# Kernel optimization log

Hardware: AMD Instinct MI355X
Metric: run time of the kernel (lower is better)

Reference implementation:

```python
import jax, jax.numpy as jnp
import numpy as np

B, S, D, H, C, E, V = 8, 2048, 1024, 512, 256, 64, 64


def setup_inputs() -> dict:
    key = jax.random.key(0)
    ks = jax.random.split(key, 40)
    ri = lambda i, hi: jax.random.randint(ks[i], (B, S), 0, hi).astype(jnp.int32)
    p = lambda i, shape: (jax.random.normal(ks[i], shape, jnp.float32) * 0.02)
    inp = {
        'h_x': jax.random.normal(ks[0], (B, S, D), jnp.float32),
        'h_y': jax.random.normal(ks[1], (B, S, D), jnp.float32),
        'x_mask': jnp.ones((B, S), jnp.int32),
        'y_mask': jnp.ones((B, S), jnp.int32),
        'src_token_dense_mask': ri(2, 2), 'src_token_sparse_mask': ri(3, 2),
        'src_token_inarc_type': ri(4, V), 'src_token_arc_head': ri(5, S),
        'src_token_depth': ri(6, 16), 'src_word_inarc_type': ri(7, V),
        'src_word_inarc_type_mask': ri(8, 2),
        'tgt_token_dense_mask': ri(9, 2), 'tgt_token_sparse_mask': ri(10, 2),
        'tgt_token_inarc_type': ri(11, V), 'tgt_token_arc_head': ri(12, S),
        'tgt_token_depth': ri(13, 16), 'tgt_word_inarc_type': ri(14, V),
        'tgt_word_inarc_type_mask': ri(15, 2),
        # src MLP [D->H->C], tgt MLP [D->H->C]
        'W1s': p(16, (D, H)), 'b1s': jnp.zeros((H,), jnp.float32),
        'W2s': p(17, (H, C)), 'b2s': jnp.zeros((C,), jnp.float32),
        'W1t': p(18, (D, H)), 'b1t': jnp.zeros((H,), jnp.float32),
        'W2t': p(19, (H, C)), 'b2t': jnp.zeros((C,), jnp.float32),
        # inarc edge embedding + GeneralConv params
        'emb': p(20, (V, E)),
        'W_msg': p(21, (C, C)), 'b_msg': jnp.zeros((C,), jnp.float32),
        'W_edge': p(22, (E, C)),
        'att': p(23, (C,)),
        'W_self': p(24, (C, C)), 'b_self': jnp.zeros((C,), jnp.float32),
        # axis_feature MLP [C->C]
        'Wf': p(25, (C, C)), 'bf': jnp.zeros((C,), jnp.float32),
    }
    return inp


def _mlp(h, W1, b1, W2, b2):
    return jax.nn.leaky_relu(h @ W1 + b1) @ W2 + b2


def _graph_side(h, dense_m, sparse_m, arc_head, word_type, word_mask,
                W1, b1, W2, b2, emb, W_msg, b_msg, W_edge, att, W_self, b_self, Wf, bf):
    Bn, Sn, _ = h.shape
    x = _mlp(h, W1, b1, W2, b2)                      # [B,S,C]
    N = Bn * Sn
    Cn = x.shape[-1]
    xg = x.reshape(N, Cn)                            # debatch -> nodes
    off = (jnp.arange(Bn, dtype=jnp.int32) * Sn)[:, None]
    src = (arc_head + off).reshape(N)                # global head index per token
    dst = jnp.arange(N, dtype=jnp.int32)             # one in-edge per token
    valid = (sparse_m * dense_m).reshape(N).astype(x.dtype)
    ef = emb[(word_type * word_mask).reshape(N)]     # [N,E] edge embeddings
    # GeneralConv: directed message with edge features + additive attention
    m = xg[src] @ W_msg + b_msg + ef @ W_edge        # [N,C] messages
    hd = xg @ W_msg + b_msg                          # dst-side term for attention
    logit = jax.nn.leaky_relu(((m + hd) * att).sum(-1))
    logit = jnp.where(valid > 0, logit, -1e9)
    emax = jax.ops.segment_max(logit, dst, num_segments=N)
    ex = jnp.exp(logit - emax[dst]) * valid
    den = jax.ops.segment_sum(ex, dst, num_segments=N)
    alpha = ex / (den[dst] + 1e-16)                  # softmax per destination node
    agg = jax.ops.segment_sum(m * alpha[:, None], dst, num_segments=N)
    out = xg @ W_self + b_self + agg                 # skip_linear
    out = out / jnp.maximum(jnp.linalg.norm(out, axis=-1, keepdims=True), 1e-12)
    r = out.reshape(Bn, Sn, Cn).mean(axis=1, keepdims=True)  # FeatureRepr mean
    return r @ Wf + bf                               # [B,1,C]


def reference(h_x, x_mask, src_token_dense_mask, src_token_sparse_mask,
              src_token_inarc_type, src_token_arc_head, src_token_depth,
              src_word_inarc_type, src_word_inarc_type_mask,
              h_y, y_mask, tgt_token_dense_mask, tgt_token_sparse_mask,
              tgt_token_inarc_type, tgt_token_arc_head, tgt_token_depth,
              tgt_word_inarc_type, tgt_word_inarc_type_mask,
              W1s, b1s, W2s, b2s, W1t, b1t, W2t, b2t,
              emb, W_msg, b_msg, W_edge, att, W_self, b_self, Wf, bf):
    src_repr = _graph_side(h_x, src_token_dense_mask, src_token_sparse_mask,
                           src_token_arc_head, src_word_inarc_type, src_word_inarc_type_mask,
                           W1s, b1s, W2s, b2s, emb, W_msg, b_msg, W_edge, att,
                           W_self, b_self, Wf, bf)
    tgt_repr = _graph_side(h_y, tgt_token_dense_mask, tgt_token_sparse_mask,
                           tgt_token_arc_head, tgt_word_inarc_type, tgt_word_inarc_type_mask,
                           W1t, b1t, W2t, b2t, emb, W_msg, b_msg, W_edge, att,
                           W_self, b_self, Wf, bf)
    return (src_repr, tgt_repr)
```

## Files before the change

kernel.cpp:

```cpp
#include <hip/hip_runtime.h>
#include <stdint.h>

#define SEQ   2048
#define NNODE 16384

typedef short  short8  __attribute__((ext_vector_type(8)));
typedef float  float4v __attribute__((ext_vector_type(4)));
typedef unsigned short u16;
typedef unsigned short u16x8 __attribute__((ext_vector_type(8)));
typedef short  short4v __attribute__((ext_vector_type(4)));

__device__ __forceinline__ float b2f(u16 u) {
    union { unsigned int i; float f; } x; x.i = ((unsigned int)u) << 16; return x.f;
}
__device__ __forceinline__ u16 f2b(float f) {
    union { float f; unsigned int i; } x; x.f = f;
    unsigned int u = x.i;
    unsigned int r = (u + 0x7fffu + ((u >> 16) & 1u)) >> 16;
    return (u16)r;
}

__device__ __forceinline__ void gld16(const void* g, void* l) {
    __builtin_amdgcn_global_load_lds(
        (const __attribute__((address_space(1))) void*)g,
        (__attribute__((address_space(3))) void*)l, 16, 0, 0);
}

struct GemmP {
    const void*  A[2];
    const u16*   B[2];
    const float* bias[2];
    u16*         out[2];
};

#define LDW 136

template <int ACT, int AF32>
__global__ __launch_bounds__(256, 2) void gemm_k(GemmP p, int M, int N, int K) {
    __shared__ __align__(16) u16 smem[32768];

    const int z = blockIdx.z;
    const u16*   __restrict__ B    = p.B[z];
    const float* __restrict__ bias = p.bias[z];
    const u16*   __restrict__ A16  = (const u16*)p.A[z];
    const float* __restrict__ A32  = (const float*)p.A[z];

    const int mt  = blockIdx.x * 128;
    const int nt  = blockIdx.y * 128;
    const int tid = threadIdx.x;
    const int l   = tid & 63;
    const int w   = tid >> 6;
    const int wm  = (w >> 1) * 64;
    const int wn  = (w & 1) * 64;
    const int lr  = l & 15;
    const int lk  = l >> 4;

    float4v acc[4][4] = {};
    float4v pa[8];

    auto stageB = [&](int k0, u16* Bs) {
#pragma unroll
        for (int it = 0; it < 4; ++it) {
            int f = it * 256 + tid, rm = f >> 3, cc = f & 7, gc = cc ^ (rm & 7);
            gld16(B + (size_t)(nt + rm) * K + (k0 + gc * 8), Bs + (size_t)f * 8);
        }
    };
    auto stageA16 = [&](int k0, u16* As) {
#pragma unroll
        for (int it = 0; it < 4; ++it) {
            int f = it * 256 + tid, rm = f >> 3, cc = f & 7, gc = cc ^ (rm & 7);
            gld16(A16 + (size_t)(mt + rm) * K + (k0 + gc * 8), As + (size_t)f * 8);
        }
    };
    auto prefA32 = [&](int k0) {
#pragma unroll
        for (int it = 0; it < 4; ++it) {
            int f = it * 256 + tid, rm = f >> 3, cc = f & 7;
            const float* s = A32 + (size_t)(mt + rm) * K + k0 + cc * 8;
            pa[2 * it]     = *(const float4v*)s;
            pa[2 * it + 1] = *(const float4v*)(s + 4);
        }
    };
    auto cvtWrite = [&](u16* As) {
#pragma unroll
        for (int it = 0; it < 4; ++it) {
            int f = it * 256 + tid, rm = f >> 3, cc = f & 7;
            float4v a = pa[2 * it], b = pa[2 * it + 1];
            u16x8 r;
            r[0] = f2b(a[0]); r[1] = f2b(a[1]); r[2] = f2b(a[2]); r[3] = f2b(a[3]);
            r[4] = f2b(b[0]); r[5] = f2b(b[1]); r[6] = f2b(b[2]); r[7] = f2b(b[3]);
            *(u16x8*)(As + ((size_t)rm * 8 + (cc ^ (rm & 7))) * 8) = r;
        }
    };

    const int niter = K >> 6;

    if (AF32) { prefA32(0); cvtWrite(smem); }
    else      { stageA16(0, smem); }
    stageB(0, smem + 8192);
    __syncthreads();

    for (int ki = 0; ki < niter; ++ki) {
        u16* curb = smem + (ki & 1) * 16384;
        u16* nxtb = smem + ((ki & 1) ^ 1) * 16384;
        const bool more = (ki + 1) < niter;
        if (more) {
            if (AF32) prefA32((ki + 1) * 64);
            else      stageA16((ki + 1) * 64, nxtb);
            stageB((ki + 1) * 64, nxtb + 8192);
        }
        const u16* As = curb;
        const u16* Bs = curb + 8192;
#pragma unroll
        for (int ks = 0; ks < 2; ++ks) {
            short8 af[4], bfr[4];
            const int kc = ks * 4 + lk;
#pragma unroll
            for (int i = 0; i < 4; ++i) {
                int ra = wm + i * 16 + lr;
                af[i]  = *(const short8*)(As + ((size_t)ra * 8 + (kc ^ (ra & 7))) * 8);
                int rb = wn + i * 16 + lr;
                bfr[i] = *(const short8*)(Bs + ((size_t)rb * 8 + (kc ^ (rb & 7))) * 8);
            }
#pragma unroll
            for (int i = 0; i < 4; ++i)
#pragma unroll
                for (int j = 0; j < 4; ++j)
                    acc[i][j] = __builtin_amdgcn_mfma_f32_16x16x32_bf16(
                        af[i], bfr[j], acc[i][j], 0, 0, 0);
        }
        if (AF32 && more) cvtWrite(nxtb);
        __syncthreads();
    }

    const int r0 = lk * 4;
#pragma unroll
    for (int j = 0; j < 4; ++j) {
        const int lc = wn + j * 16 + lr;
        const float bv = bias[nt + lc];
#pragma unroll
        for (int i = 0; i < 4; ++i) {
            const int lrow = wm + i * 16 + r0;
#pragma unroll
            for (int r = 0; r < 4; ++r) {
                float v = acc[i][j][r] + bv;
                if (ACT) v = v > 0.f ? v : 0.01f * v;
                smem[(size_t)(lrow + r) * LDW + lc] = f2b(v);
            }
        }
    }
    __syncthreads();
#pragma unroll
    for (int pass = 0; pass < 8; ++pass) {
        int id  = pass * 256 + tid;
        int row = id >> 4, colc = id & 15;
        u16x8 vv = *(const u16x8*)(smem + (size_t)row * LDW + colc * 8);
        *(u16x8*)(p.out[z] + (size_t)(mt + row) * N + nt + colc * 8) = vv;
    }
}

struct TP { const float* src[6]; u16* dst[6]; int K[6]; int N[6]; };

__global__ __launch_bounds__(256) void transpose_k(TP t) {
    __shared__ float tile[64][65];
    const int m = blockIdx.y;
    const int K = t.K[m], N = t.N[m];
    const int tn = N >> 6;
    const int ntiles = (K >> 6) * tn;
    const int bid = blockIdx.x;
    if (bid >= ntiles) return;
    const int k0 = (bid / tn) * 64, n0 = (bid % tn) * 64;
    const int tid = threadIdx.x;
#pragma unroll
    for (int pass = 0; pass < 4; ++pass) {
        int kk = pass * 16 + (tid >> 4);
        int nn = (tid & 15) * 4;
        float4v v = *(const float4v*)(t.src[m] + (size_t)(k0 + kk) * N + n0 + nn);
        tile[kk][nn + 0] = v[0]; tile[kk][nn + 1] = v[1];
        tile[kk][nn + 2] = v[2]; tile[kk][nn + 3] = v[3];
    }
    __syncthreads();
    const int n = tid >> 2, kc = (tid & 3) * 16;
    u16x8 a, b;
#pragma unroll
    for (int j = 0; j < 8; ++j) {
        a[j] = f2b(tile[kc + j][n]);
        b[j] = f2b(tile[kc + 8 + j][n]);
    }
    u16* d = t.dst[m] + (size_t)(n0 + n) * K + k0 + kc;
    *(u16x8*)d = a;
    *(u16x8*)(d + 8) = b;
}

__global__ void ew_k(const float* emb, const float* W_edge, float* EW) {
    const int t = blockIdx.x, c = threadIdx.x;
    float s = 0.f;
    for (int e = 0; e < 64; ++e)
        s += emb[t * 64 + e] * W_edge[e * 256 + c];
    EW[t * 256 + c] = s;
}

__global__ void bias_cat_k(const float* bmsg, const float* bself, float* bcat) {
    const int tid = threadIdx.x;
    bcat[tid]       = bmsg[tid];
    bcat[256 + tid] = bself[tid];
}

struct EpiP {
    const u16* xcat[2];
    const int* den[2]; const int* spa[2]; const int* arc[2];
    const int* wty[2]; const int* wma[2];
    const float* EW; float* racc;
};

__global__ __launch_bounds__(256) void epi_k(EpiP p) {
    __shared__ float part[4][256];
    const int bx    = blockIdx.x;
    const int side  = bx >> 9;
    const int local = bx & 511;
    const int base  = local * 32;
    const int b     = base >> 11;
    const int tid   = threadIdx.x;
    const int w = tid >> 6, l = tid & 63;

    const u16* __restrict__ xcat = p.xcat[side];

    float4v acc = {};
    for (int j = 0; j < 8; ++j) {
        const int i     = base + w * 8 + j;
        const int valid = p.den[side][i] * p.spa[side][i];
        const int srcn  = p.arc[side][i] + (i >> 11) * SEQ;
        const int t     = p.wty[side][i] * p.wma[side][i];
        short4v xs = *(const short4v*)(xcat + (size_t)i * 512 + 256 + l * 4);
        short4v xm = *(const short4v*)(xcat + (size_t)srcn * 512 + l * 4);
        float4v ew = *(const float4v*)(p.EW + (size_t)t * 256 + l * 4);
        const float vm = valid ? 1.f : 0.f;
        float4v v;
        v[0] = b2f((u16)xs[0]) + vm * (b2f((u16)xm[0]) + ew[0]);
        v[1] = b2f((u16)xs[1]) + vm * (b2f((u16)xm[1]) + ew[1]);
        v[2] = b2f((u16)xs[2]) + vm * (b2f((u16)xm[2]) + ew[2]);
        v[3] = b2f((u16)xs[3]) + vm * (b2f((u16)xm[3]) + ew[3]);
        float ss = v[0]*v[0] + v[1]*v[1] + v[2]*v[2] + v[3]*v[3];
        for (int m = 32; m >= 1; m >>= 1) ss += __shfl_xor(ss, m, 64);
        const float rn = 1.f / fmaxf(sqrtf(ss), 1e-12f);
        acc[0] += v[0] * rn; acc[1] += v[1] * rn;
        acc[2] += v[2] * rn; acc[3] += v[3] * rn;
    }
    part[w][l * 4 + 0] = acc[0];
    part[w][l * 4 + 1] = acc[1];
    part[w][l * 4 + 2] = acc[2];
    part[w][l * 4 + 3] = acc[3];
    __syncthreads();
    const float s = part[0][tid] + part[1][tid] + part[2][tid] + part[3][tid];
    atomicAdd(p.racc + ((size_t)side * 8 + b) * 256 + tid, s);
}

__global__ void fin_k(const float* racc, const float* Wf, const float* bfv,
                      float* out) {
    __shared__ float r[256];
    const int bid = blockIdx.x;
    const int tid = threadIdx.x;
    r[tid] = racc[bid * 256 + tid] * (1.f / 2048.f);
    __syncthreads();
    float s = bfv[tid];
    for (int k = 0; k < 256; ++k)
        s += r[k] * Wf[k * 256 + tid];
    out[bid * 256 + tid] = s;
}

extern "C" void kernel_launch(void* const* d_in, const int* in_sizes, int n_in,
                              void* d_out, int out_size, void* d_ws, size_t ws_size,
                              hipStream_t stream) {
    const float* h[2]   = {(const float*)d_in[0],  (const float*)d_in[1]};
    const int* den[2]   = {(const int*)d_in[4],  (const int*)d_in[11]};
    const int* spa[2]   = {(const int*)d_in[5],  (const int*)d_in[12]};
    const int* arc[2]   = {(const int*)d_in[7],  (const int*)d_in[14]};
    const int* wty[2]   = {(const int*)d_in[9],  (const int*)d_in[16]};
    const int* wma[2]   = {(const int*)d_in[10], (const int*)d_in[17]};
    const float* W1[2]  = {(const float*)d_in[18], (const float*)d_in[22]};
    const float* b1[2]  = {(const float*)d_in[19], (const float*)d_in[23]};
    const float* W2[2]  = {(const float*)d_in[20], (const float*)d_in[24]};
    const float* b2[2]  = {(const float*)d_in[21], (const float*)d_in[25]};
    const float* emb    = (const float*)d_in[26];
    const float* Wmsg   = (const float*)d_in[27];
    const float* bmsg   = (const float*)d_in[28];
    const float* Wedge  = (const float*)d_in[29];
    const float* Wself  = (const float*)d_in[31];
    const float* bself  = (const float*)d_in[32];
    const float* Wf     = (const float*)d_in[33];
    const float* bf_    = (const float*)d_in[34];

    char* ws = (char*)d_ws;
    size_t off = 0;
    auto alloc = [&](size_t bytes) -> void* {
        void* pp = ws + off; off += (bytes + 255) & ~(size_t)255; return pp;
    };
    u16*   x1    = (u16*)  alloc(2ull * NNODE * 512 * 2);
    u16*   xx    = (u16*)  alloc(2ull * NNODE * 256 * 2);
    u16*   xcat  = (u16*)  alloc(2ull * NNODE * 512 * 2);
    u16*   W1T   = (u16*)  alloc(2ull * 512 * 1024 * 2);
    u16*   W2T   = (u16*)  alloc(2ull * 256 * 512 * 2);
    u16*   WcatT = (u16*)  alloc(512 * 256 * 2);
    float* EW    = (float*)alloc(64 * 256 * 4);
    float* bcat  = (float*)alloc(512 * 4);
    float* racc  = (float*)alloc(2 * 8 * 256 * 4);

    TP tp;
    tp.src[0] = W1[0]; tp.dst[0] = W1T;              tp.K[0] = 1024; tp.N[0] = 512;
    tp.src[1] = W1[1]; tp.dst[1] = W1T + 512 * 1024; tp.K[1] = 1024; tp.N[1] = 512;
    tp.src[2] = W2[0]; tp.dst[2] = W2T;              tp.K[2] = 512;  tp.N[2] = 256;
    tp.src[3] = W2[1]; tp.dst[3] = W2T + 256 * 512;  tp.K[3] = 512;  tp.N[3] = 256;
    tp.src[4] = Wmsg;  tp.dst[4] = WcatT;            tp.K[4] = 256;  tp.N[4] = 256;
    tp.src[5] = Wself; tp.dst[5] = WcatT + 256*256;  tp.K[5] = 256;  tp.N[5] = 256;
    hipLaunchKernelGGL(transpose_k, dim3(128, 6), dim3(256), 0, stream, tp);
    hipLaunchKernelGGL(ew_k, dim3(64), dim3(256), 0, stream, emb, Wedge, EW);
    hipLaunchKernelGGL(bias_cat_k, dim3(1), dim3(256), 0, stream, bmsg, bself, bcat);
    hipMemsetAsync(racc, 0, 2 * 8 * 256 * 4, stream);

    GemmP g1 = {};
    g1.A[0] = h[0];  g1.A[1] = h[1];
    g1.B[0] = W1T;   g1.B[1] = W1T + 512 * 1024;
    g1.bias[0] = b1[0]; g1.bias[1] = b1[1];
    g1.out[0] = x1;  g1.out[1] = x1 + (size_t)NNODE * 512;
    hipLaunchKernelGGL((gemm_k<1, 1>), dim3(128, 4, 2), dim3(256), 0, stream,
                       g1, NNODE, 512, 1024);

    GemmP g2 = {};
    g2.A[0] = x1;  g2.A[1] = x1 + (size_t)NNODE * 512;
    g2.B[0] = W2T; g2.B[1] = W2T + 256 * 512;
    g2.bias[0] = b2[0]; g2.bias[1] = b2[1];
    g2.out[0] = xx; g2.out[1] = xx + (size_t)NNODE * 256;
    hipLaunchKernelGGL((gemm_k<0, 0>), dim3(128, 2, 2), dim3(256), 0, stream,
                       g2, NNODE, 256, 512);

    GemmP g3 = {};
    g3.A[0] = xx;    g3.A[1] = xx + (size_t)NNODE * 256;
    g3.B[0] = WcatT; g3.B[1] = WcatT;
    g3.bias[0] = bcat; g3.bias[1] = bcat;
    g3.out[0] = xcat;  g3.out[1] = xcat + (size_t)NNODE * 512;
    hipLaunchKernelGGL((gemm_k<0, 0>), dim3(128, 4, 2), dim3(256), 0, stream,
                       g3, NNODE, 512, 256);

    EpiP ep;
    ep.xcat[0] = xcat; ep.xcat[1] = xcat + (size_t)NNODE * 512;
    for (int s = 0; s < 2; ++s) {
        ep.den[s] = den[s]; ep.spa[s] = spa[s]; ep.arc[s] = arc[s];
        ep.wty[s] = wty[s]; ep.wma[s] = wma[s];
    }
    ep.EW = EW; ep.racc = racc;
    hipLaunchKernelGGL(epi_k, dim3(1024), dim3(256), 0, stream, ep);

    hipLaunchKernelGGL(fin_k, dim3(16), dim3(256), 0, stream,
                       racc, Wf, bf_, (float*)d_out);
}
```

Before: 310.6 us.

## Rewrite GEMM as 256x256 eight-wave tile with triple-buffered interleaved pipeline

Replaces the 128x128 four-wave GEMM with a 256x256 tile computed by eight waves over a K=32 step. Loads go into a triple-buffered LDS ring, and each tile is split into two MFMA halves separated by explicit barriers, s_setprio and manual waitcnt, so global loads and fp32-to-bf16 conversion overlap with compute. The larger tile raises data reuse per loaded byte. In exchange it uses more LDS and registers and launches fewer blocks (256 or 128 per GEMM), which may underfill the GPU. The hand-tuned vmcnt counts are fragile.

```diff
diff --git a/kernel.cpp b/kernel.cpp
--- a/kernel.cpp
+++ b/kernel.cpp
@@ -33,129 +33,171 @@
     u16*         out[2];
 };
 
-#define LDW 136
+template <int MB>
+__device__ __forceinline__ void mfma4(const short8* af, const short8* bq,
+                                      float4v (*acc)[4]) {
+#pragma unroll
+    for (int mi = 0; mi < 4; ++mi)
+#pragma unroll
+        for (int ni = 0; ni < 4; ++ni)
+            acc[MB + mi][ni] = __builtin_amdgcn_mfma_f32_16x16x32_bf16(
+                af[mi], bq[ni], acc[MB + mi][ni], 0, 0, 0);
+}
+
+#define TILE_BODY(AC, BC, KN, AG, BG, ACV, PL, PC)                            \
+    {                                                                         \
+        short8 bq[4], af[4];                                                  \
+        _Pragma("unroll") for (int ni = 0; ni < 4; ++ni)                      \
+            bq[ni] = *(const short8*)((BC) + boff + ni * 512);                \
+        _Pragma("unroll") for (int mi = 0; mi < 4; ++mi)                      \
+            af[mi] = *(const short8*)((AC) + aoff + mi * 512);                \
+        if constexpr (AF32) prefA32(KN, PL); else stageA16(KN, AG);           \
+        __builtin_amdgcn_s_barrier();                                         \
+        __builtin_amdgcn_s_setprio(1);                                        \
+        mfma4<0>(af, bq, acc);                                                \
+        __builtin_amdgcn_s_setprio(0);                                        \
+        __builtin_amdgcn_s_barrier();                                         \
+        _Pragma("unroll") for (int mi = 0; mi < 4; ++mi)                      \
+            af[mi] = *(const short8*)((AC) + aoff + (4 + mi) * 512);          \
+        stageB(KN, BG);                                                       \
+        if constexpr (AF32) {                                                 \
+            cvtWrite(PC, ACV);                                                \
+            asm volatile("s_waitcnt lgkmcnt(0)" ::: "memory");                \
+            asm volatile("s_waitcnt vmcnt(6)" ::: "memory");                  \
+        } else {                                                              \
+            asm volatile("s_waitcnt vmcnt(4)" ::: "memory");                  \
+        }                                                                     \
+        __builtin_amdgcn_s_barrier();                                         \
+        __builtin_amdgcn_s_setprio(1);                                        \
+        mfma4<4>(af, bq, acc);                                                \
+        __builtin_amdgcn_s_setprio(0);                                        \
+        __builtin_amdgcn_s_barrier();                                         \
+    }
 
 template <int ACT, int AF32>
-__global__ __launch_bounds__(256, 2) void gemm_k(GemmP p, int M, int N, int K) {
-    __shared__ __align__(16) u16 smem[32768];
+__global__ __launch_bounds__(512, 2) void gemm8_k(GemmP p, int M, int N, int K) {
+    __shared__ __align__(16) u16 smem[49152];
 
     const int z = blockIdx.z;
-    const u16*   __restrict__ B    = p.B[z];
+    const u16*   __restrict__ Bg   = p.B[z];
     const float* __restrict__ bias = p.bias[z];
     const u16*   __restrict__ A16  = (const u16*)p.A[z];
     const float* __restrict__ A32  = (const float*)p.A[z];
 
-    const int mt  = blockIdx.x * 128;
-    const int nt  = blockIdx.y * 128;
+    const int mt  = blockIdx.x * 256;
+    const int nt  = blockIdx.y * 256;
     const int tid = threadIdx.x;
     const int l   = tid & 63;
     const int w   = tid >> 6;
-    const int wm  = (w >> 1) * 64;
-    const int wn  = (w & 1) * 64;
+    const int wm  = (w >> 2) * 128;
+    const int wn  = (w & 3) * 64;
     const int lr  = l & 15;
     const int lk  = l >> 4;
-
-    float4v acc[4][4] = {};
-    float4v pa[8];
-
-    auto stageB = [&](int k0, u16* Bs) {
-#pragma unroll
-        for (int it = 0; it < 4; ++it) {
-            int f = it * 256 + tid, rm = f >> 3, cc = f & 7, gc = cc ^ (rm & 7);
-            gld16(B + (size_t)(nt + rm) * K + (k0 + gc * 8), Bs + (size_t)f * 8);
+    (void)M;
+
+    float4v acc[8][4] = {};
+    float4v paA[4], paB[4];
+
+    const int rm0 = tid >> 2;
+    const int cc0 = tid & 3;
+    const int gc0 = cc0 ^ (rm0 & 3) ^ ((rm0 >> 2) & 3);
+    const int rm1 = rm0 + 128;
+
+    u16* const As0 = smem;
+    u16* const Bs0 = smem + 24576;
+
+    auto stageA16 = [&](int k0, u16* dst) {
+        gld16(A16 + (size_t)(mt + rm0) * K + k0 + gc0 * 8, dst + tid * 8);
+        gld16(A16 + (size_t)(mt + rm1) * K + k0 + gc0 * 8, dst + (tid + 512) * 8);
+    };
+    auto stageB = [&](int k0, u16* dst) {
+        gld16(Bg + (size_t)(nt + rm0) * K + k0 + gc0 * 8, dst + tid * 8);
+        gld16(Bg + (size_t)(nt + rm1) * K + k0 + gc0 * 8, dst + (tid + 512) * 8);
+    };
+    auto prefA32 = [&](int k0, float4v* pa) {
+        const float* s0 = A32 + (size_t)(mt + rm0) * K + k0 + gc0 * 8;
+        const float* s1 = A32 + (size_t)(mt + rm1) * K + k0 + gc0 * 8;
+        pa[0] = *(const float4v*)s0; pa[1] = *(const float4v*)(s0 + 4);
+        pa[2] = *(const float4v*)s1; pa[3] = *(const float4v*)(s1 + 4);
+    };
+    auto cvtWrite = [&](const float4v* pa, u16* dst) {
+        u16x8 r0, r1;
+        r0[0]=f2b(pa[0][0]); r0[1]=f2b(pa[0][1]); r0[2]=f2b(pa[0][2]); r0[3]=f2b(pa[0][3]);
+        r0[4]=f2b(pa[1][0]); r0[5]=f2b(pa[1][1]); r0[6]=f2b(pa[1][2]); r0[7]=f2b(pa[1][3]);
+        r1[0]=f2b(pa[2][0]); r1[1]=f2b(pa[2][1]); r1[2]=f2b(pa[2][2]); r1[3]=f2b(pa[2][3]);
+        r1[4]=f2b(pa[3][0]); r1[5]=f2b(pa[3][1]); r1[6]=f2b(pa[3][2]); r1[7]=f2b(pa[3][3]);
+        *(u16x8*)(dst + tid * 8) = r0;
+        *(u16x8*)(dst + (tid + 512) * 8) = r1;
+    };
+
+    const int fsl  = lk ^ (lr & 3) ^ ((lr >> 2) & 3);
+    const int aoff = (wm + lr) * 32 + fsl * 8;
+    const int boff = (wn + lr) * 32 + fsl * 8;
+
+    const int KT = K >> 5;
+
+    if constexpr (AF32) {
+        float4v p0[4];
+        prefA32(0, p0);
+        stageB(0, Bs0);
+        prefA32(32, paB);
+        stageB(32, Bs0 + 8192);
+        cvtWrite(p0, As0);
+        asm volatile("s_waitcnt lgkmcnt(0)" ::: "memory");
+        asm volatile("s_waitcnt vmcnt(6)" ::: "memory");
+    } else {
+        stageA16(0, As0);          stageB(0, Bs0);
+        stageA16(32, As0 + 8192);  stageB(32, Bs0 + 8192);
+        asm volatile("s_waitcnt vmcnt(4)" ::: "memory");
+    }
+    __builtin_amdgcn_s_barrier();
+
+    int sc = 0;
+    for (int kt = 0; kt < KT; kt += 2) {
+        const int sc1 = (sc == 2) ? 0 : sc + 1;
+        const int sc2 = (sc1 == 2) ? 0 : sc1 + 1;
+        u16* Ae = As0 + sc  * 8192;  u16* Be = Bs0 + sc  * 8192;
+        u16* Ao = As0 + sc1 * 8192;  u16* Bo = Bs0 + sc1 * 8192;
+        u16* A2 = As0 + sc2 * 8192;  u16* B2 = Bs0 + sc2 * 8192;
+        const int k2 = (kt + 2 < KT) ? (kt + 2) << 5 : 0;
+        const int k3 = (kt + 3 < KT) ? (kt + 3) << 5 : 0;
+        TILE_BODY(Ae, Be, k2, A2, B2, Ao, paA, paB)
+        TILE_BODY(Ao, Bo, k3, Ae, Be, A2, paB, paA)
+        sc = sc2;
+    }
+
+    __syncthreads();
+
+    const int r0 = lk * 4;
+    float bvv[4];
+#pragma unroll
+    for (int ni = 0; ni < 4; ++ni) bvv[ni] = bias[nt + wn + ni * 16 + lr];
+    const int half = w >> 2;
+#pragma unroll
+    for (int pass = 0; pass < 2; ++pass) {
+        if (half == pass) {
+#pragma unroll
+            for (int mi = 0; mi < 8; ++mi)
+#pragma unroll
+                for (int ni = 0; ni < 4; ++ni) {
+                    const int lc = wn + ni * 16 + lr;
+#pragma unroll
+                    for (int r = 0; r < 4; ++r) {
+                        float v = acc[mi][ni][r] + bvv[ni];
+                        if (ACT) v = v > 0.f ? v : 0.01f * v;
+                        smem[(mi * 16 + r0 + r) * 264 + lc] = f2b(v);
+                    }
+                }
         }
-    };
-    auto stageA16 = [&](int k0, u16* As) {
-#pragma unroll
-        for (int it = 0; it < 4; ++it) {
-            int f = it * 256 + tid, rm = f >> 3, cc = f & 7, gc = cc ^ (rm & 7);
-            gld16(A16 + (size_t)(mt + rm) * K + (k0 + gc * 8), As + (size_t)f * 8);
+        __syncthreads();
+#pragma unroll
+        for (int it = 0; it < 8; ++it) {
+            const int id  = it * 512 + tid;
+            const int row = id >> 5, colc = id & 31;
+            u16x8 vv = *(const u16x8*)(smem + (size_t)row * 264 + colc * 8);
+            *(u16x8*)(p.out[z] + (size_t)(mt + pass * 128 + row) * N + nt + colc * 8) = vv;
         }
-    };
-    auto prefA32 = [&](int k0) {
-#pragma unroll
-        for (int it = 0; it < 4; ++it) {
-            int f = it * 256 + tid, rm = f >> 3, cc = f & 7;
-            const float* s = A32 + (size_t)(mt + rm) * K + k0 + cc * 8;
-            pa[2 * it]     = *(const float4v*)s;
-            pa[2 * it + 1] = *(const float4v*)(s + 4);
-        }
-    };
-    auto cvtWrite = [&](u16* As) {
-#pragma unroll
-        for (int it = 0; it < 4; ++it) {
-            int f = it * 256 + tid, rm = f >> 3, cc = f & 7;
-            float4v a = pa[2 * it], b = pa[2 * it + 1];
-            u16x8 r;
-            r[0] = f2b(a[0]); r[1] = f2b(a[1]); r[2] = f2b(a[2]); r[3] = f2b(a[3]);
-            r[4] = f2b(b[0]); r[5] = f2b(b[1]); r[6] = f2b(b[2]); r[7] = f2b(b[3]);
-            *(u16x8*)(As + ((size_t)rm * 8 + (cc ^ (rm & 7))) * 8) = r;
-        }
-    };
-
-    const int niter = K >> 6;
-
-    if (AF32) { prefA32(0); cvtWrite(smem); }
-    else      { stageA16(0, smem); }
-    stageB(0, smem + 8192);
-    __syncthreads();
-
-    for (int ki = 0; ki < niter; ++ki) {
-        u16* curb = smem + (ki & 1) * 16384;
-        u16* nxtb = smem + ((ki & 1) ^ 1) * 16384;
-        const bool more = (ki + 1) < niter;
-        if (more) {
-            if (AF32) prefA32((ki + 1) * 64);
-            else      stageA16((ki + 1) * 64, nxtb);
-            stageB((ki + 1) * 64, nxtb + 8192);
-        }
-        const u16* As = curb;
-        const u16* Bs = curb + 8192;
-#pragma unroll
-        for (int ks = 0; ks < 2; ++ks) {
-            short8 af[4], bfr[4];
-            const int kc = ks * 4 + lk;
-#pragma unroll
-            for (int i = 0; i < 4; ++i) {
-                int ra = wm + i * 16 + lr;
-                af[i]  = *(const short8*)(As + ((size_t)ra * 8 + (kc ^ (ra & 7))) * 8);
-                int rb = wn + i * 16 + lr;
-                bfr[i] = *(const short8*)(Bs + ((size_t)rb * 8 + (kc ^ (rb & 7))) * 8);
-            }
-#pragma unroll
-            for (int i = 0; i < 4; ++i)
-#pragma unroll
-                for (int j = 0; j < 4; ++j)
-                    acc[i][j] = __builtin_amdgcn_mfma_f32_16x16x32_bf16(
-                        af[i], bfr[j], acc[i][j], 0, 0, 0);
-        }
-        if (AF32 && more) cvtWrite(nxtb);
         __syncthreads();
-    }
-
-    const int r0 = lk * 4;
-#pragma unroll
-    for (int j = 0; j < 4; ++j) {
-        const int lc = wn + j * 16 + lr;
-        const float bv = bias[nt + lc];
-#pragma unroll
-        for (int i = 0; i < 4; ++i) {
-            const int lrow = wm + i * 16 + r0;
-#pragma unroll
-            for (int r = 0; r < 4; ++r) {
-                float v = acc[i][j][r] + bv;
-                if (ACT) v = v > 0.f ? v : 0.01f * v;
-                smem[(size_t)(lrow + r) * LDW + lc] = f2b(v);
-            }
-        }
-    }
-    __syncthreads();
-#pragma unroll
-    for (int pass = 0; pass < 8; ++pass) {
-        int id  = pass * 256 + tid;
-        int row = id >> 4, colc = id & 15;
-        u16x8 vv = *(const u16x8*)(smem + (size_t)row * LDW + colc * 8);
-        *(u16x8*)(p.out[z] + (size_t)(mt + row) * N + nt + colc * 8) = vv;
     }
 }
 
@@ -322,7 +364,7 @@
     g1.B[0] = W1T;   g1.B[1] = W1T + 512 * 1024;
     g1.bias[0] = b1[0]; g1.bias[1] = b1[1];
     g1.out[0] = x1;  g1.out[1] = x1 + (size_t)NNODE * 512;
-    hipLaunchKernelGGL((gemm_k<1, 1>), dim3(128, 4, 2), dim3(256), 0, stream,
+    hipLaunchKernelGGL((gemm8_k<1, 1>), dim3(64, 2, 2), dim3(512), 0, stream,
                        g1, NNODE, 512, 1024);
 
     GemmP g2 = {};
@@ -330,7 +372,7 @@
     g2.B[0] = W2T; g2.B[1] = W2T + 256 * 512;
     g2.bias[0] = b2[0]; g2.bias[1] = b2[1];
     g2.out[0] = xx; g2.out[1] = xx + (size_t)NNODE * 256;
-    hipLaunchKernelGGL((gemm_k<0, 0>), dim3(128, 2, 2), dim3(256), 0, stream,
+    hipLaunchKernelGGL((gemm8_k<0, 0>), dim3(64, 1, 2), dim3(512), 0, stream,
                        g2, NNODE, 256, 512);
 
     GemmP g3 = {};
@@ -338,7 +380,7 @@
     g3.B[0] = WcatT; g3.B[1] = WcatT;
     g3.bias[0] = bcat; g3.bias[1] = bcat;
     g3.out[0] = xcat;  g3.out[1] = xcat + (size_t)NNODE * 512;
-    hipLaunchKernelGGL((gemm_k<0, 0>), dim3(128, 4, 2), dim3(256), 0, stream,
+    hipLaunchKernelGGL((gemm8_k<0, 0>), dim3(64, 2, 2), dim3(512), 0, stream,
                        g3, NNODE, 512, 256);
 
     EpiP ep;
```

Measured after the change: 301.8 us. 2.9% less time.
